# Kernel tuning notes

Measured on AMD Instinct MI355X. Metric: run time of the kernel, lower is better.

## Reference

```python
import jax, jax.numpy as jnp
import numpy as np

KH, KW = 3, 3
STRIDE = (1, 1)
PAD = (1, 1)
DIL = (1, 1)
DG = 1  # num_deformable_groups


def _out_size(h, pad, dil, k, stride):
    return (h + 2 * pad - (dil * (k - 1) + 1)) // stride + 1


def setup_inputs() -> dict:
    key = jax.random.key(0)
    k1, k2, k3 = jax.random.split(key, 3)
    B, Cin, H, W = 8, 128, 64, 64
    Cout = 128
    Ho = _out_size(H, PAD[0], DIL[0], KH, STRIDE[0])
    Wo = _out_size(W, PAD[1], DIL[1], KW, STRIDE[1])
    x = jax.random.normal(k1, (B, Cin, H, W), jnp.float32)
    offset = jax.random.normal(k2, (B, 2 * DG * KH * KW, Ho, Wo), jnp.float32)
    n = Cin * KH * KW
    stdv = 1.0 / np.sqrt(n)
    weight = jax.random.uniform(k3, (Cout, Cin, KH, KW), jnp.float32, -stdv, stdv)
    return {"x": x, "offset": offset, "weight": weight}


def deform_conv2d(x, offset, weight):
    B, Cin, H, W = x.shape
    Cout, _, kh, kw = weight.shape
    K = kh * kw
    Ho = _out_size(H, PAD[0], DIL[0], kh, STRIDE[0])
    Wo = _out_size(W, PAD[1], DIL[1], kw, STRIDE[1])
    G = DG
    Cg = Cin // G

    # base sampling grid per kernel tap: [kh,kw,Ho,Wo]
    by = (jnp.arange(kh) * DIL[0])[:, None, None, None] + (jnp.arange(Ho) * STRIDE[0] - PAD[0])[None, None, :, None]
    bx = (jnp.arange(kw) * DIL[1])[None, :, None, None] + (jnp.arange(Wo) * STRIDE[1] - PAD[1])[None, None, None, :]
    by = jnp.broadcast_to(by, (kh, kw, Ho, Wo)).reshape(K, Ho, Wo).astype(x.dtype)
    bx = jnp.broadcast_to(bx, (kh, kw, Ho, Wo)).reshape(K, Ho, Wo).astype(x.dtype)

    # offset layout: channel = g*2*K + 2*k + {0: dy, 1: dx}
    off = offset.reshape(B, G, K, 2, Ho, Wo)
    py = by[None, None] + off[:, :, :, 0]  # [B,G,K,Ho,Wo]
    px = bx[None, None] + off[:, :, :, 1]

    y0 = jnp.floor(py).astype(jnp.int32)
    x0 = jnp.floor(px).astype(jnp.int32)
    wy = (py - y0).reshape(B, G, 1, -1)  # fractional parts, [B,G,1,K*Ho*Wo]
    wx = (px - x0).reshape(B, G, 1, -1)

    xg = x.reshape(B, G, Cg, H * W)
    N = K * Ho * Wo

    def gather(yi, xi):
        valid = ((yi >= 0) & (yi < H) & (xi >= 0) & (xi < W)).reshape(B, G, 1, N)
        idx = (jnp.clip(yi, 0, H - 1) * W + jnp.clip(xi, 0, W - 1)).reshape(B, G, 1, N)
        v = jnp.take_along_axis(xg, jnp.broadcast_to(idx, (B, G, Cg, N)), axis=3)
        return v * valid.astype(x.dtype)

    v00 = gather(y0, x0)
    v01 = gather(y0, x0 + 1)
    v10 = gather(y0 + 1, x0)
    v11 = gather(y0 + 1, x0 + 1)

    cols = (v00 * (1 - wy) * (1 - wx) + v01 * (1 - wy) * wx
            + v10 * wy * (1 - wx) + v11 * wy * wx)
    cols = cols.reshape(B, G, Cg, K, Ho, Wo)  # deformable im2col columns

    wr = weight.reshape(Cout, G, Cg, K)
    return jnp.einsum('ogck,bgcknm->bonm', wr, cols)


def reference(x, offset, weight):
    return deform_conv2d(x, offset, weight)
```

## Files before the change

### kernel.cpp

```cpp
#include <hip/hip_runtime.h>
#include <hip/hip_fp16.h>

typedef __attribute__((ext_vector_type(4))) float f32x4;
typedef __attribute__((ext_vector_type(8))) _Float16 f16x8;
typedef __attribute__((ext_vector_type(4))) unsigned int u32x4;

__device__ __forceinline__ unsigned short f2h(float f) {
  __half h = __float2half_rn(f);
  unsigned short u;
  __builtin_memcpy(&u, &h, 2);
  return u;
}
__device__ __forceinline__ __half2 h2_of(unsigned int u) {
  __half2 h;
  __builtin_memcpy(&h, &u, 4);
  return h;
}
__device__ __forceinline__ unsigned int u_of(__half2 h) {
  unsigned int u;
  __builtin_memcpy(&u, &h, 4);
  return u;
}

__global__ __launch_bounds__(256) void prep_kernel(const float* __restrict__ w,
                                                   unsigned short* __restrict__ wf) {
  int tid = blockIdx.x * 256 + threadIdx.x;
  int l  = tid & 63;
  int mt = (tid >> 6) & 7;
  int ch = tid >> 9;
  int cc = ch / 9, tap = ch - cc * 9;
  int co = mt * 16 + (l & 15);
  int cb = cc * 32 + (l >> 4) * 8;
  unsigned int r[8];
#pragma unroll
  for (int j = 0; j < 8; ++j)
    r[j] = f2h(w[(co * 128 + cb + j) * 9 + tap]);
  u32x4 pk;
  pk.x = r[0] | (r[1] << 16);
  pk.y = r[2] | (r[3] << 16);
  pk.z = r[4] | (r[5] << 16);
  pk.w = r[6] | (r[7] << 16);
  *reinterpret_cast<u32x4*>(wf + (size_t)tid * 8) = pk;
}

__global__ __launch_bounds__(512, 1) void deform_kernel(const float* __restrict__ x,
                                                        const float* __restrict__ off,
                                                        const unsigned short* __restrict__ wf,
                                                        float* __restrict__ out) {
  __shared__ __align__(16) unsigned char sWin[8 * 17408];
  __shared__ int4 sTab[1152];

  const int tid = threadIdx.x;
  const int bid = blockIdx.x;
  const int b   = bid & 7;
  const int ho0 = (bid >> 3) * 2;
  const int r0  = min(max(ho0 - 3, 0), 56);

  {
    const float* xb = x + ((size_t)b << 19) + ((size_t)r0 << 6);
#pragma unroll
    for (int it = 0; it < 16; ++it) {
      int idx = it * 512 + tid;
      int p  = idx & 63;
      int r  = (idx >> 6) & 7;
      int cg = idx >> 9;
      const float* xp = xb + (((size_t)cg) << 15) + (r << 6) + p;
      unsigned int q[8];
#pragma unroll
      for (int j = 0; j < 8; ++j) q[j] = f2h(xp[(size_t)j << 12]);
      u32x4 pk;
      pk.x = q[0] | (q[1] << 16);
      pk.y = q[2] | (q[3] << 16);
      pk.z = q[4] | (q[5] << 16);
      pk.w = q[6] | (q[7] << 16);
      *reinterpret_cast<u32x4*>(&sWin[r * 17408 + p * 272 + cg * 16]) = pk;
    }
  }

  for (int r = tid; r < 1152; r += 512) {
    int row = (r >= 576) ? 1 : 0;
    int rr  = r - row * 576;
    int tap = rr >> 6, wo = rr & 63;
    int ho = ho0 + row;
    float dy = off[((b * 18 + 2 * tap)     * 64 + ho) * 64 + wo];
    float dx = off[((b * 18 + 2 * tap + 1) * 64 + ho) * 64 + wo];
    float py = (float)(ho + (tap / 3) - 1) + dy;
    float px = (float)(wo + (tap % 3) - 1) + dx;
    float fy = floorf(py), fx = floorf(px);
    int y0 = (int)fy, x0 = (int)fx;
    float wy = py - fy, wx = px - fx;
    float wt = (y0 >= 0 && y0 < 64) ? (1.f - wy) : 0.f;
    float wb = (y0 + 1 >= 0 && y0 + 1 < 64) ? wy : 0.f;
    int y0c = min(max(y0, 0), 63), y1c = min(max(y0 + 1, 0), 63);
    int bx; float wl, wr;
    if (x0 >= 0 && x0 <= 62)      { bx = x0; wl = 1.f - wx; wr = wx;       }
    else if (x0 == -1)            { bx = 0;  wl = wx;       wr = 0.f;      }
    else if (x0 == 63)            { bx = 62; wl = 0.f;      wr = 1.f - wx; }
    else                          { bx = 0;  wl = 0.f;      wr = 0.f;      }
    int aX = y0c * 64 + bx, aY = y1c * 64 + bx;
    int twr = y0c - r0, bwr = y1c - r0;
    int tin = ((unsigned)twr < 8u) ? 1 : 0;
    int bin = ((unsigned)bwr < 8u) ? 1 : 0;
    int laT0 = (tin ? twr : 0) * 17408 + bx * 272;
    int laB0 = (bin ? bwr : 0) * 17408 + bx * 272;
    int4 pw;
    pw.x = laT0 | (aX << 18) | (tin ? 0 : (int)0x80000000);
    pw.y = laB0 | (aY << 18) | (bin ? 0 : (int)0x80000000);
    pw.z = (int)u_of(__floats2half2_rn(wt * wl, wt * wr));
    pw.w = (int)u_of(__floats2half2_rn(wb * wl, wb * wr));
    sTab[r] = pw;
  }
  __syncthreads();

  const int l   = tid & 63;
  const int w   = tid >> 6;
  const int ks  = w & 3;
  const int row = w >> 2;
  const int ln  = l & 15;
  const int kg  = l >> 4;
  const int koff = ks * 64 + kg * 16;
  const int ho  = ho0 + row;
  const int tbase = row * 576 + ln;

  const float* xfb = x + ((size_t)b << 19) + (((size_t)(ks * 32 + kg * 8)) << 12);
  const unsigned short* wfb = wf + (size_t)l * 8;

  f32x4 acc[4][8] = {};

  int4 tbc[4];
#pragma unroll
  for (int pg = 0; pg < 4; ++pg) tbc[pg] = sTab[tbase + pg * 16];

#define ISSUE(S, PG) {                                                         \
    const int4 tb = tbc[PG];                                                   \
    const int laT = (tb.x & 0x3FFFF) + koff;                                   \
    __builtin_memcpy(&T0[S], &sWin[laT],       16);                            \
    __builtin_memcpy(&T1[S], &sWin[laT + 272], 16);                            \
    const int laB = (tb.y & 0x3FFFF) + koff;                                   \
    __builtin_memcpy(&B0[S], &sWin[laB],       16);                            \
    __builtin_memcpy(&B1[S], &sWin[laB + 272], 16);                            \
    if (tb.x < 0) {    \
      const float* p0 = xfb + ((tb.x >> 18) & 4095);                           \
      u32x4 q0, q1;                                                            \
      _Pragma("unroll") for (int d = 0; d < 4; ++d) {                          \
        unsigned int a0 = f2h(p0[(size_t)(2 * d)     << 12]);                  \
        unsigned int a1 = f2h(p0[(size_t)(2 * d + 1) << 12]);                  \
        q0[d] = a0 | (a1 << 16);                                               \
        unsigned int c0 = f2h(p0[((size_t)(2 * d)     << 12) + 1]);            \
        unsigned int c1 = f2h(p0[((size_t)(2 * d + 1) << 12) + 1]);            \
        q1[d] = c0 | (c1 << 16);                                               \
      }                                                                        \
      T0[S] = q0; T1[S] = q1;                                                  \
    }                                                                          \
    if (tb.y < 0) {                \
      const float* p1 = xfb + ((tb.y >> 18) & 4095);                           \
      u32x4 q0, q1;                                                            \
      _Pragma("unroll") for (int d = 0; d < 4; ++d) {                          \
        unsigned int a0 = f2h(p1[(size_t)(2 * d)     << 12]);                  \
        unsigned int a1 = f2h(p1[(size_t)(2 * d + 1) << 12]);                  \
        q0[d] = a0 | (a1 << 16);                                               \
        unsigned int c0 = f2h(p1[((size_t)(2 * d)     << 12) + 1]);            \
        unsigned int c1 = f2h(p1[((size_t)(2 * d + 1) << 12) + 1]);            \
        q1[d] = c0 | (c1 << 16);                                               \
      }                                                                        \
      B0[S] = q0; B1[S] = q1;                                                  \
    }                                                                          \
  }

#define INTERP(S, PG) {                                                        \
    const __half2 wtl = __half2half2(__low2half(h2_of((unsigned)tbc[PG].z)));  \
    const __half2 wtr = __half2half2(__high2half(h2_of((unsigned)tbc[PG].z))); \
    const __half2 wbl = __half2half2(__low2half(h2_of((unsigned)tbc[PG].w)));  \
    const __half2 wbr = __half2half2(__high2half(h2_of((unsigned)tbc[PG].w))); \
    u32x4 pk;                                                                  \
    _Pragma("unroll") for (int d = 0; d < 4; ++d) {                            \
      __half2 s = __hmul2(wtl, h2_of(T0[S][d]));                               \
      s = __hfma2(wtr, h2_of(T1[S][d]), s);                                    \
      s = __hfma2(wbl, h2_of(B0[S][d]), s);                                    \
      s = __hfma2(wbr, h2_of(B1[S][d]), s);                                    \
      pk[d] = u_of(s);                                                         \
    }                                                                          \
    f16x8 bfrag;                                                               \
    __builtin_memcpy(&bfrag, &pk, 16);                                         \
    _Pragma("unroll") for (int mt = 0; mt < 8; ++mt)                           \
      acc[PG][mt] = __builtin_amdgcn_mfma_f32_16x16x32_f16(A[mt], bfrag,       \
                                                           acc[PG][mt], 0, 0, 0); \
  }

  for (int tap = 0; tap < 9; ++tap) {
    int4 tbn[4];
    if (tap < 8) {
#pragma unroll
      for (int pg = 0; pg < 4; ++pg)
        tbn[pg] = sTab[tbase + (tap + 1) * 64 + pg * 16];
    }

    f16x8 A[8];
    const unsigned short* wp = wfb + (size_t)((ks * 9 + tap) * 8) * 512;
#pragma unroll
    for (int mt = 0; mt < 8; ++mt)
      A[mt] = *reinterpret_cast<const f16x8*>(wp + (size_t)mt * 512);

    u32x4 T0[3], T1[3], B0[3], B1[3];
    ISSUE(0, 0)
    ISSUE(1, 1)
    ISSUE(2, 2)
    INTERP(0, 0)
    ISSUE(0, 3)
    INTERP(1, 1)
    INTERP(2, 2)
    INTERP(0, 3)

#pragma unroll
    for (int pg = 0; pg < 4; ++pg) tbc[pg] = tbn[pg];
  }
#undef ISSUE
#undef INTERP

  float* sF = reinterpret_cast<float*>(sWin);
#define WR_LDS(BASE)                                                           \
  { _Pragma("unroll") for (int pg = 0; pg < 4; ++pg)                           \
    _Pragma("unroll") for (int mt = 0; mt < 8; ++mt)                           \
      *reinterpret_cast<f32x4*>(&sF[(BASE) + row * 8448 + (pg * 16 + ln) * 132 + mt * 16 + kg * 4]) = acc[pg][mt]; }
#define RD_LDS(BASE)                                                           \
  { _Pragma("unroll") for (int pg = 0; pg < 4; ++pg)                           \
    _Pragma("unroll") for (int mt = 0; mt < 8; ++mt) {                         \
      f32x4 v = *reinterpret_cast<const f32x4*>(&sF[(BASE) + row * 8448 + (pg * 16 + ln) * 132 + mt * 16 + kg * 4]); \
      acc[pg][mt] += v; } }

  __syncthreads();
  if (ks == 1) WR_LDS(17408)
  if (ks == 3) WR_LDS(0)
  __syncthreads();
  if (ks == 0) RD_LDS(17408)
  if (ks == 2) RD_LDS(0)
  __syncthreads();
  if (ks == 2) WR_LDS(17408)
  __syncthreads();
  if (ks == 0) RD_LDS(17408)
#undef WR_LDS
#undef RD_LDS

  {
    const int b2 = row * 8704;
    if (ks == 0) {
#pragma unroll
      for (int pg = 0; pg < 4; ++pg)
#pragma unroll
        for (int mt = 0; mt < 8; ++mt)
#pragma unroll
          for (int rg = 0; rg < 4; ++rg)
            sF[b2 + (mt * 16 + kg * 4 + rg) * 68 + pg * 16 + ln] = acc[pg][mt][rg];
    }
    __syncthreads();
    if (ks == 0) {
      const int q4  = l & 15;
      const int ch2 = l >> 4;
      float* ob = out + (((size_t)b * 128) * 64 + ho) * 64 + q4 * 4;
#pragma unroll
      for (int i = 0; i < 32; ++i) {
        int co = ch2 * 32 + i;
        f32x4 v = *reinterpret_cast<const f32x4*>(&sF[b2 + co * 68 + q4 * 4]);
        *reinterpret_cast<f32x4*>(ob + (size_t)co * 4096) = v;
      }
    }
  }
}

extern "C" void kernel_launch(void* const* d_in, const int* in_sizes, int n_in,
                              void* d_out, int out_size, void* d_ws, size_t ws_size,
                              hipStream_t stream) {
  (void)in_sizes; (void)n_in; (void)out_size; (void)ws_size;
  const float* x   = (const float*)d_in[0];
  const float* off = (const float*)d_in[1];
  const float* w   = (const float*)d_in[2];
  float* out = (float*)d_out;
  unsigned short* wf = (unsigned short*)d_ws;

  prep_kernel<<<72, 256, 0, stream>>>(w, wf);
  deform_kernel<<<256, 512, 0, stream>>>(x, off, wf, out);
}
```

Baseline: 96.58 us.

## Precompute sampling table in prep kernel and use butterfly split-K reduction

```diff
diff --git a/kernel.cpp b/kernel.cpp
--- a/kernel.cpp
+++ b/kernel.cpp
@@ -23,65 +23,38 @@
 }
 
 __global__ __launch_bounds__(256) void prep_kernel(const float* __restrict__ w,
-                                                   unsigned short* __restrict__ wf) {
-  int tid = blockIdx.x * 256 + threadIdx.x;
-  int l  = tid & 63;
-  int mt = (tid >> 6) & 7;
-  int ch = tid >> 9;
-  int cc = ch / 9, tap = ch - cc * 9;
-  int co = mt * 16 + (l & 15);
-  int cb = cc * 32 + (l >> 4) * 8;
-  unsigned int r[8];
-#pragma unroll
-  for (int j = 0; j < 8; ++j)
-    r[j] = f2h(w[(co * 128 + cb + j) * 9 + tap]);
-  u32x4 pk;
-  pk.x = r[0] | (r[1] << 16);
-  pk.y = r[2] | (r[3] << 16);
-  pk.z = r[4] | (r[5] << 16);
-  pk.w = r[6] | (r[7] << 16);
-  *reinterpret_cast<u32x4*>(wf + (size_t)tid * 8) = pk;
-}
-
-__global__ __launch_bounds__(512, 1) void deform_kernel(const float* __restrict__ x,
-                                                        const float* __restrict__ off,
-                                                        const unsigned short* __restrict__ wf,
-                                                        float* __restrict__ out) {
-  __shared__ __align__(16) unsigned char sWin[8 * 17408];
-  __shared__ int4 sTab[1152];
-
-  const int tid = threadIdx.x;
-  const int bid = blockIdx.x;
-  const int b   = bid & 7;
-  const int ho0 = (bid >> 3) * 2;
-  const int r0  = min(max(ho0 - 3, 0), 56);
-
-  {
-    const float* xb = x + ((size_t)b << 19) + ((size_t)r0 << 6);
-#pragma unroll
-    for (int it = 0; it < 16; ++it) {
-      int idx = it * 512 + tid;
-      int p  = idx & 63;
-      int r  = (idx >> 6) & 7;
-      int cg = idx >> 9;
-      const float* xp = xb + (((size_t)cg) << 15) + (r << 6) + p;
-      unsigned int q[8];
-#pragma unroll
-      for (int j = 0; j < 8; ++j) q[j] = f2h(xp[(size_t)j << 12]);
-      u32x4 pk;
-      pk.x = q[0] | (q[1] << 16);
-      pk.y = q[2] | (q[3] << 16);
-      pk.z = q[4] | (q[5] << 16);
-      pk.w = q[6] | (q[7] << 16);
-      *reinterpret_cast<u32x4*>(&sWin[r * 17408 + p * 272 + cg * 16]) = pk;
-    }
-  }
-
-  for (int r = tid; r < 1152; r += 512) {
-    int row = (r >= 576) ? 1 : 0;
-    int rr  = r - row * 576;
-    int tap = rr >> 6, wo = rr & 63;
-    int ho = ho0 + row;
+                                                   const float* __restrict__ off,
+                                                   unsigned short* __restrict__ wf,
+                                                   int4* __restrict__ tab) {
+  if (blockIdx.x < 72) {
+    int tid = blockIdx.x * 256 + threadIdx.x;
+    int l  = tid & 63;
+    int mt = (tid >> 6) & 7;
+    int ch = tid >> 9;
+    int cc = ch / 9, tap = ch - cc * 9;
+    int co = mt * 16 + (l & 15);
+    int cb = cc * 32 + (l >> 4) * 8;
+    unsigned int r[8];
+#pragma unroll
+    for (int j = 0; j < 8; ++j)
+      r[j] = f2h(w[(co * 128 + cb + j) * 9 + tap]);
+    u32x4 pk;
+    pk.x = r[0] | (r[1] << 16);
+    pk.y = r[2] | (r[3] << 16);
+    pk.z = r[4] | (r[5] << 16);
+    pk.w = r[6] | (r[7] << 16);
+    *reinterpret_cast<u32x4*>(wf + (size_t)tid * 8) = pk;
+  } else {
+    int t = (blockIdx.x - 72) * 256 + threadIdx.x;
+    int wo  = t & 63;
+    int q   = t >> 6;
+    int tap = q % 9;
+    int rest = q / 9;
+    int ho  = rest & 63;
+    int b   = rest >> 6;
+    int ho0 = ho & ~1;
+    int r0  = min(max(ho0 - 3, 0), 56);
+
     float dy = off[((b * 18 + 2 * tap)     * 64 + ho) * 64 + wo];
     float dx = off[((b * 18 + 2 * tap + 1) * 64 + ho) * 64 + wo];
     float py = (float)(ho + (tap / 3) - 1) + dy;
@@ -108,9 +81,21 @@
     pw.y = laB0 | (aY << 18) | (bin ? 0 : (int)0x80000000);
     pw.z = (int)u_of(__floats2half2_rn(wt * wl, wt * wr));
     pw.w = (int)u_of(__floats2half2_rn(wb * wl, wb * wr));
-    sTab[r] = pw;
-  }
-  __syncthreads();
+    tab[t] = pw;
+  }
+}
+
+__global__ __launch_bounds__(512, 1) void deform_kernel(const float* __restrict__ x,
+                                                        const int4* __restrict__ tab,
+                                                        const unsigned short* __restrict__ wf,
+                                                        float* __restrict__ out) {
+  __shared__ __align__(16) unsigned char sWin[8 * 17408];
+
+  const int tid = threadIdx.x;
+  const int bid = blockIdx.x;
+  const int b   = bid & 7;
+  const int ho0 = (bid >> 3) * 2;
+  const int r0  = min(max(ho0 - 3, 0), 56);
 
   const int l   = tid & 63;
   const int w   = tid >> 6;
@@ -120,16 +105,39 @@
   const int kg  = l >> 4;
   const int koff = ks * 64 + kg * 16;
   const int ho  = ho0 + row;
-  const int tbase = row * 576 + ln;
+
+  const int4* tabp = tab + (size_t)((b * 64 + ho) * 9) * 64 + ln;
+
+  int4 tbc[4];
+#pragma unroll
+  for (int pg = 0; pg < 4; ++pg) tbc[pg] = tabp[pg * 16];
+
+  {
+    const float* xb = x + ((size_t)b << 19) + ((size_t)r0 << 6);
+#pragma unroll
+    for (int it = 0; it < 16; ++it) {
+      int idx = it * 512 + tid;
+      int p  = idx & 63;
+      int r  = (idx >> 6) & 7;
+      int cg = idx >> 9;
+      const float* xp = xb + (((size_t)cg) << 15) + (r << 6) + p;
+      unsigned int q[8];
+#pragma unroll
+      for (int j = 0; j < 8; ++j) q[j] = f2h(xp[(size_t)j << 12]);
+      u32x4 pk;
+      pk.x = q[0] | (q[1] << 16);
+      pk.y = q[2] | (q[3] << 16);
+      pk.z = q[4] | (q[5] << 16);
+      pk.w = q[6] | (q[7] << 16);
+      *reinterpret_cast<u32x4*>(&sWin[r * 17408 + p * 272 + cg * 16]) = pk;
+    }
+  }
+  __syncthreads();
 
   const float* xfb = x + ((size_t)b << 19) + (((size_t)(ks * 32 + kg * 8)) << 12);
   const unsigned short* wfb = wf + (size_t)l * 8;
 
   f32x4 acc[4][8] = {};
-
-  int4 tbc[4];
-#pragma unroll
-  for (int pg = 0; pg < 4; ++pg) tbc[pg] = sTab[tbase + pg * 16];
 
 #define ISSUE(S, PG) {                                                         \
     const int4 tb = tbc[PG];                                                   \
@@ -192,7 +200,7 @@
     if (tap < 8) {
 #pragma unroll
       for (int pg = 0; pg < 4; ++pg)
-        tbn[pg] = sTab[tbase + (tap + 1) * 64 + pg * 16];
+        tbn[pg] = tabp[(tap + 1) * 64 + pg * 16];
     }
 
     f16x8 A[8];
@@ -217,53 +225,57 @@
 #undef ISSUE
 #undef INTERP
 
-  float* sF = reinterpret_cast<float*>(sWin);
-#define WR_LDS(BASE)                                                           \
-  { _Pragma("unroll") for (int pg = 0; pg < 4; ++pg)                           \
-    _Pragma("unroll") for (int mt = 0; mt < 8; ++mt)                           \
-      *reinterpret_cast<f32x4*>(&sF[(BASE) + row * 8448 + (pg * 16 + ln) * 132 + mt * 16 + kg * 4]) = acc[pg][mt]; }
-#define RD_LDS(BASE)                                                           \
-  { _Pragma("unroll") for (int pg = 0; pg < 4; ++pg)                           \
-    _Pragma("unroll") for (int mt = 0; mt < 8; ++mt) {                         \
-      f32x4 v = *reinterpret_cast<const f32x4*>(&sF[(BASE) + row * 8448 + (pg * 16 + ln) * 132 + mt * 16 + kg * 4]); \
-      acc[pg][mt] += v; } }
-
-  __syncthreads();
-  if (ks == 1) WR_LDS(17408)
-  if (ks == 3) WR_LDS(0)
-  __syncthreads();
-  if (ks == 0) RD_LDS(17408)
-  if (ks == 2) RD_LDS(0)
-  __syncthreads();
-  if (ks == 2) WR_LDS(17408)
-  __syncthreads();
-  if (ks == 0) RD_LDS(17408)
-#undef WR_LDS
-#undef RD_LDS
-
   {
-    const int b2 = row * 8704;
-    if (ks == 0) {
-#pragma unroll
-      for (int pg = 0; pg < 4; ++pg)
-#pragma unroll
-        for (int mt = 0; mt < 8; ++mt)
-#pragma unroll
-          for (int rg = 0; rg < 4; ++rg)
-            sF[b2 + (mt * 16 + kg * 4 + rg) * 68 + pg * 16 + ln] = acc[pg][mt][rg];
-    }
-    __syncthreads();
-    if (ks == 0) {
-      const int q4  = l & 15;
-      const int ch2 = l >> 4;
-      float* ob = out + (((size_t)b * 128) * 64 + ho) * 64 + q4 * 4;
-#pragma unroll
-      for (int i = 0; i < 32; ++i) {
-        int co = ch2 * 32 + i;
-        f32x4 v = *reinterpret_cast<const f32x4*>(&sF[b2 + co * 68 + q4 * 4]);
-        *reinterpret_cast<f32x4*>(ob + (size_t)co * 4096) = v;
+    float* sF = reinterpret_cast<float*>(sWin);
+    const int rbase = w * 4352;
+    const int pbase1 = (w ^ 1) * 4352;
+    const int pbase2 = (w ^ 2) * 4352;
+    const int sendB  = (ks & 1) ? 0 : 4;
+    const int keepB  = 4 - sendB;
+    const int send2B = keepB + ((ks >> 1) ? 0 : 2);
+    const int keep2B = keepB + ((ks >> 1) ? 2 : 0);
+
+    __syncthreads();
+#pragma unroll
+    for (int pg = 0; pg < 4; ++pg)
+#pragma unroll
+      for (int mtL = 0; mtL < 4; ++mtL)
+        *reinterpret_cast<f32x4*>(&sF[rbase + (pg * 16 + ln) * 68 + mtL * 16 + kg * 4]) = acc[pg][sendB + mtL];
+    __syncthreads();
+#pragma unroll
+    for (int pg = 0; pg < 4; ++pg)
+#pragma unroll
+      for (int mtL = 0; mtL < 4; ++mtL) {
+        f32x4 v = *reinterpret_cast<const f32x4*>(&sF[pbase1 + (pg * 16 + ln) * 68 + mtL * 16 + kg * 4]);
+        acc[pg][keepB + mtL] += v;
       }
-    }
+    __syncthreads();
+#pragma unroll
+    for (int pg = 0; pg < 4; ++pg)
+#pragma unroll
+      for (int mtL = 0; mtL < 2; ++mtL)
+        *reinterpret_cast<f32x4*>(&sF[rbase + (pg * 16 + ln) * 68 + mtL * 16 + kg * 4]) = acc[pg][send2B + mtL];
+    __syncthreads();
+#pragma unroll
+    for (int pg = 0; pg < 4; ++pg)
+#pragma unroll
+      for (int mtL = 0; mtL < 2; ++mtL) {
+        f32x4 v = *reinterpret_cast<const f32x4*>(&sF[pbase2 + (pg * 16 + ln) * 68 + mtL * 16 + kg * 4]);
+        acc[pg][keep2B + mtL] += v;
+      }
+
+    float* ob = out + (((size_t)b * 128) * 64 + ho) * 64;
+#pragma unroll
+    for (int pg = 0; pg < 4; ++pg)
+#pragma unroll
+      for (int mtL = 0; mtL < 2; ++mtL) {
+        const int mt = keep2B + mtL;
+#pragma unroll
+        for (int rg = 0; rg < 4; ++rg) {
+          const int co = mt * 16 + kg * 4 + rg;
+          ob[(size_t)co * 4096 + pg * 16 + ln] = acc[pg][mt][rg];
+        }
+      }
   }
 }
 
@@ -276,7 +288,8 @@
   const float* w   = (const float*)d_in[2];
   float* out = (float*)d_out;
   unsigned short* wf = (unsigned short*)d_ws;
-
-  prep_kernel<<<72, 256, 0, stream>>>(w, wf);
-  deform_kernel<<<256, 512, 0, stream>>>(x, off, wf, out);
-}
+  int4* tab = (int4*)((char*)d_ws + 294912);
+
+  prep_kernel<<<1224, 256, 0, stream>>>(w, off, wf, tab);
+  deform_kernel<<<256, 512, 0, stream>>>(x, tab, wf, out);
+}
```

After: 127.5 us. 32.0% more time.

## Precompute bilinear sampling table in prep kernel and read from global memory

Applied to the files above, without the earlier changes.

```diff
diff --git a/kernel.cpp b/kernel.cpp
--- a/kernel.cpp
+++ b/kernel.cpp
@@ -23,65 +23,38 @@
 }
 
 __global__ __launch_bounds__(256) void prep_kernel(const float* __restrict__ w,
-                                                   unsigned short* __restrict__ wf) {
-  int tid = blockIdx.x * 256 + threadIdx.x;
-  int l  = tid & 63;
-  int mt = (tid >> 6) & 7;
-  int ch = tid >> 9;
-  int cc = ch / 9, tap = ch - cc * 9;
-  int co = mt * 16 + (l & 15);
-  int cb = cc * 32 + (l >> 4) * 8;
-  unsigned int r[8];
-#pragma unroll
-  for (int j = 0; j < 8; ++j)
-    r[j] = f2h(w[(co * 128 + cb + j) * 9 + tap]);
-  u32x4 pk;
-  pk.x = r[0] | (r[1] << 16);
-  pk.y = r[2] | (r[3] << 16);
-  pk.z = r[4] | (r[5] << 16);
-  pk.w = r[6] | (r[7] << 16);
-  *reinterpret_cast<u32x4*>(wf + (size_t)tid * 8) = pk;
-}
-
-__global__ __launch_bounds__(512, 1) void deform_kernel(const float* __restrict__ x,
-                                                        const float* __restrict__ off,
-                                                        const unsigned short* __restrict__ wf,
-                                                        float* __restrict__ out) {
-  __shared__ __align__(16) unsigned char sWin[8 * 17408];
-  __shared__ int4 sTab[1152];
-
-  const int tid = threadIdx.x;
-  const int bid = blockIdx.x;
-  const int b   = bid & 7;
-  const int ho0 = (bid >> 3) * 2;
-  const int r0  = min(max(ho0 - 3, 0), 56);
-
-  {
-    const float* xb = x + ((size_t)b << 19) + ((size_t)r0 << 6);
-#pragma unroll
-    for (int it = 0; it < 16; ++it) {
-      int idx = it * 512 + tid;
-      int p  = idx & 63;
-      int r  = (idx >> 6) & 7;
-      int cg = idx >> 9;
-      const float* xp = xb + (((size_t)cg) << 15) + (r << 6) + p;
-      unsigned int q[8];
-#pragma unroll
-      for (int j = 0; j < 8; ++j) q[j] = f2h(xp[(size_t)j << 12]);
-      u32x4 pk;
-      pk.x = q[0] | (q[1] << 16);
-      pk.y = q[2] | (q[3] << 16);
-      pk.z = q[4] | (q[5] << 16);
-      pk.w = q[6] | (q[7] << 16);
-      *reinterpret_cast<u32x4*>(&sWin[r * 17408 + p * 272 + cg * 16]) = pk;
-    }
-  }
-
-  for (int r = tid; r < 1152; r += 512) {
-    int row = (r >= 576) ? 1 : 0;
-    int rr  = r - row * 576;
-    int tap = rr >> 6, wo = rr & 63;
-    int ho = ho0 + row;
+                                                   const float* __restrict__ off,
+                                                   unsigned short* __restrict__ wf,
+                                                   int4* __restrict__ tab) {
+  if (blockIdx.x < 72) {
+    int tid = blockIdx.x * 256 + threadIdx.x;
+    int l  = tid & 63;
+    int mt = (tid >> 6) & 7;
+    int ch = tid >> 9;
+    int cc = ch / 9, tap = ch - cc * 9;
+    int co = mt * 16 + (l & 15);
+    int cb = cc * 32 + (l >> 4) * 8;
+    unsigned int r[8];
+#pragma unroll
+    for (int j = 0; j < 8; ++j)
+      r[j] = f2h(w[(co * 128 + cb + j) * 9 + tap]);
+    u32x4 pk;
+    pk.x = r[0] | (r[1] << 16);
+    pk.y = r[2] | (r[3] << 16);
+    pk.z = r[4] | (r[5] << 16);
+    pk.w = r[6] | (r[7] << 16);
+    *reinterpret_cast<u32x4*>(wf + (size_t)tid * 8) = pk;
+  } else {
+    int t = (blockIdx.x - 72) * 256 + threadIdx.x;
+    int wo  = t & 63;
+    int q   = t >> 6;
+    int tap = q % 9;
+    int rest = q / 9;
+    int ho  = rest & 63;
+    int b   = rest >> 6;
+    int ho0 = ho & ~1;
+    int r0  = min(max(ho0 - 3, 0), 56);
+
     float dy = off[((b * 18 + 2 * tap)     * 64 + ho) * 64 + wo];
     float dx = off[((b * 18 + 2 * tap + 1) * 64 + ho) * 64 + wo];
     float py = (float)(ho + (tap / 3) - 1) + dy;
@@ -108,9 +81,21 @@
     pw.y = laB0 | (aY << 18) | (bin ? 0 : (int)0x80000000);
     pw.z = (int)u_of(__floats2half2_rn(wt * wl, wt * wr));
     pw.w = (int)u_of(__floats2half2_rn(wb * wl, wb * wr));
-    sTab[r] = pw;
-  }
-  __syncthreads();
+    tab[t] = pw;
+  }
+}
+
+__global__ __launch_bounds__(512, 1) void deform_kernel(const float* __restrict__ x,
+                                                        const int4* __restrict__ tab,
+                                                        const unsigned short* __restrict__ wf,
+                                                        float* __restrict__ out) {
+  __shared__ __align__(16) unsigned char sWin[8 * 17408];
+
+  const int tid = threadIdx.x;
+  const int bid = blockIdx.x;
+  const int b   = bid & 7;
+  const int ho0 = (bid >> 3) * 2;
+  const int r0  = min(max(ho0 - 3, 0), 56);
 
   const int l   = tid & 63;
   const int w   = tid >> 6;
@@ -120,16 +105,39 @@
   const int kg  = l >> 4;
   const int koff = ks * 64 + kg * 16;
   const int ho  = ho0 + row;
-  const int tbase = row * 576 + ln;
+
+  const int4* tabp = tab + (size_t)((b * 64 + ho) * 9) * 64 + ln;
+
+  int4 tbc[4];
+#pragma unroll
+  for (int pg = 0; pg < 4; ++pg) tbc[pg] = tabp[pg * 16];
+
+  {
+    const float* xb = x + ((size_t)b << 19) + ((size_t)r0 << 6);
+#pragma unroll
+    for (int it = 0; it < 16; ++it) {
+      int idx = it * 512 + tid;
+      int p  = idx & 63;
+      int r  = (idx >> 6) & 7;
+      int cg = idx >> 9;
+      const float* xp = xb + (((size_t)cg) << 15) + (r << 6) + p;
+      unsigned int q[8];
+#pragma unroll
+      for (int j = 0; j < 8; ++j) q[j] = f2h(xp[(size_t)j << 12]);
+      u32x4 pk;
+      pk.x = q[0] | (q[1] << 16);
+      pk.y = q[2] | (q[3] << 16);
+      pk.z = q[4] | (q[5] << 16);
+      pk.w = q[6] | (q[7] << 16);
+      *reinterpret_cast<u32x4*>(&sWin[r * 17408 + p * 272 + cg * 16]) = pk;
+    }
+  }
+  __syncthreads();
 
   const float* xfb = x + ((size_t)b << 19) + (((size_t)(ks * 32 + kg * 8)) << 12);
   const unsigned short* wfb = wf + (size_t)l * 8;
 
   f32x4 acc[4][8] = {};
-
-  int4 tbc[4];
-#pragma unroll
-  for (int pg = 0; pg < 4; ++pg) tbc[pg] = sTab[tbase + pg * 16];
 
 #define ISSUE(S, PG) {                                                         \
     const int4 tb = tbc[PG];                                                   \
@@ -192,7 +200,7 @@
     if (tap < 8) {
 #pragma unroll
       for (int pg = 0; pg < 4; ++pg)
-        tbn[pg] = sTab[tbase + (tap + 1) * 64 + pg * 16];
+        tbn[pg] = tabp[(tap + 1) * 64 + pg * 16];
     }
 
     f16x8 A[8];
@@ -276,7 +284,8 @@
   const float* w   = (const float*)d_in[2];
   float* out = (float*)d_out;
   unsigned short* wf = (unsigned short*)d_ws;
-
-  prep_kernel<<<72, 256, 0, stream>>>(w, wf);
-  deform_kernel<<<256, 512, 0, stream>>>(x, off, wf, out);
-}
+  int4* tab = (int4*)((char*)d_ws + 294912);
+
+  prep_kernel<<<1224, 256, 0, stream>>>(w, off, wf, tab);
+  deform_kernel<<<256, 512, 0, stream>>>(x, tab, wf, out);
+}
```

Result: slower. 99.60 us (+3.1%).
